# Optimization experiments

Measured on AMD Instinct MI355X. Metric: run time of the kernel, lower is better.

The kernel has to match this reference:

```python
import jax, jax.numpy as jnp
import numpy as np

H = 2048        # hidden_size
NH = 32         # num_attention_heads
HD = H // NH    # head_dim
I = 8192        # intermediate_size
L = 2           # num_hidden_layers
B, S = 1, 2048
EPS = 1e-5


def _layernorm(x, gamma):
    # keras LayerNormalization(center=False): mean-subtract, var-normalize, scale by gamma (no beta)
    mu = jnp.mean(x, axis=-1, keepdims=True)
    var = jnp.mean(jnp.square(x - mu), axis=-1, keepdims=True)
    return (x - mu) * jax.lax.rsqrt(var + EPS) * gamma


def _gelu_tanh(x):
    return 0.5 * x * (1.0 + jnp.tanh(0.7978845608028654 * x * (1.0 + 0.044715 * x * x)))


def setup_inputs() -> dict:
    key = jax.random.key(0)
    ks = jax.random.split(key, 12)
    sd = 0.02
    inputs_embeds = jax.random.normal(ks[0], (B, S, H), dtype=jnp.float32)
    attention_mask = jnp.tril(jnp.ones((S, S), dtype=bool))[None, None]  # causal [1,1,S,S]
    return {
        "inputs_embeds": inputs_embeds,
        "attention_mask": attention_mask,
        "Wq": jax.random.normal(ks[1], (L, H, H), jnp.float32) * sd,
        "Wk": jax.random.normal(ks[2], (L, H, H), jnp.float32) * sd,
        "Wv": jax.random.normal(ks[3], (L, H, H), jnp.float32) * sd,
        "Wo": jax.random.normal(ks[4], (L, H, H), jnp.float32) * sd,
        "bo": jnp.zeros((L, H), jnp.float32),
        "W1": jax.random.normal(ks[5], (L, H, I), jnp.float32) * sd,
        "W2": jax.random.normal(ks[6], (L, I, H), jnp.float32) * sd,
        "b2": jnp.zeros((L, H), jnp.float32),
        "g1": jnp.ones((L, H), jnp.float32),
        "g2": jnp.ones((L, H), jnp.float32),
        "gf": jnp.ones((H,), jnp.float32),
    }


def _forward(inputs_embeds, attention_mask, Wq, Wk, Wv, Wo, bo, W1, W2, b2, g1, g2, gf):
    x = inputs_embeds
    scale = 1.0 / jnp.sqrt(jnp.float32(HD))
    for l in range(L):
        # --- attention block ---
        h = _layernorm(x, g1[l])
        q = h @ Wq[l]
        k = h @ Wk[l]
        v = h @ Wv[l]
        # split heads: [B,S,H] -> [B,NH,S,HD]
        q = q.reshape(B, S, NH, HD).transpose(0, 2, 1, 3)
        k = k.reshape(B, S, NH, HD).transpose(0, 2, 1, 3)
        v = v.reshape(B, S, NH, HD).transpose(0, 2, 1, 3)
        scores = jnp.einsum("bhqd,bhkd->bhqk", q, k) * scale
        scores = jnp.where(attention_mask, scores, jnp.float32(-1e9))
        probs = jax.nn.softmax(scores, axis=-1)
        ctx = jnp.einsum("bhqk,bhkd->bhqd", probs, v)
        ctx = ctx.transpose(0, 2, 1, 3).reshape(B, S, H)
        x = x + (ctx @ Wo[l] + bo[l])
        # --- MLP block ---
        h = _layernorm(x, g2[l])
        h = _gelu_tanh(h @ W1[l]) @ W2[l] + b2[l]
        x = x + h
    return _layernorm(x, gf)


def reference(inputs_embeds, attention_mask, Wq, Wk, Wv, Wo, bo, W1, W2, b2, g1, g2, gf):
    return _forward(inputs_embeds, attention_mask, Wq, Wk, Wv, Wo, bo, W1, W2, b2, g1, g2, gf)
```

## Files before the change

### kernel.cpp

```cpp
#include <hip/hip_runtime.h>
#include <hip/hip_bf16.h>
#include <stdint.h>


#define H_   2048
#define NH_  32
#define HD_  64
#define I_   8192
#define L_   2
#define S_   2048
#define EPS_ 1e-5f

typedef _Float16 f16;
typedef __attribute__((ext_vector_type(8))) _Float16 f16x8;
typedef __attribute__((ext_vector_type(4))) float   f32x4;

#define BF16_PROBE 0x3F803F80u

static __device__ __forceinline__ float bf2f(unsigned short b) {
  return __uint_as_float(((unsigned int)b) << 16);
}

static __device__ __forceinline__ float gelu_f(float x) {
  float y = 0.7978845608028654f * x * (1.0f + 0.044715f * x * x);
  return x / (1.0f + __expf(-2.0f * y));
}

#define GLDS(gp, lp)                                                          \
  __builtin_amdgcn_global_load_lds(                                           \
      (const __attribute__((address_space(1))) unsigned int*)(gp),            \
      (__attribute__((address_space(3))) unsigned int*)(lp), 16, 0, 0)

__global__ __launch_bounds__(256) void embed2f_k(const void* __restrict__ e,
                                                 float* __restrict__ xf,
                                                 const unsigned int* __restrict__ probe) {
  bool isbf = (*probe == BF16_PROBE);
  int i = (blockIdx.x * 256 + threadIdx.x) * 4;
  float4 o;
  if (isbf) {
    uint2 d = *(const uint2*)((const unsigned short*)e + i);
    o.x = bf2f((unsigned short)(d.x & 0xffff));
    o.y = bf2f((unsigned short)(d.x >> 16));
    o.z = bf2f((unsigned short)(d.y & 0xffff));
    o.w = bf2f((unsigned short)(d.y >> 16));
  } else {
    o = *(const float4*)((const float*)e + i);
  }
  *(float4*)(xf + i) = o;
}

template <int OUT_FINAL>
__global__ __launch_bounds__(256) void ln_k(const float* __restrict__ x,
                                            const void* __restrict__ gammav,
                                            size_t geoff,
                                            void* __restrict__ outv,
                                            const unsigned int* __restrict__ probe) {
  bool isbf = (*probe == BF16_PROBE);
  int row = blockIdx.x, t = threadIdx.x;
  const float* xr = x + (size_t)row * H_;
  float4 a = ((const float4*)xr)[t];
  float4 b = ((const float4*)xr)[t + 256];
  float s  = a.x + a.y + a.z + a.w + b.x + b.y + b.z + b.w;
  float ss = a.x*a.x + a.y*a.y + a.z*a.z + a.w*a.w
           + b.x*b.x + b.y*b.y + b.z*b.z + b.w*b.w;
#pragma unroll
  for (int m = 32; m >= 1; m >>= 1) { s += __shfl_xor(s, m); ss += __shfl_xor(ss, m); }
  __shared__ float red[8];
  if ((t & 63) == 0) { red[t >> 6] = s; red[4 + (t >> 6)] = ss; }
  __syncthreads();
  s  = red[0] + red[1] + red[2] + red[3];
  ss = red[4] + red[5] + red[6] + red[7];
  float mu   = s * (1.0f / H_);
  float rstd = rsqrtf(ss * (1.0f / H_) - mu * mu + EPS_);
  float va[8] = {a.x, a.y, a.z, a.w, b.x, b.y, b.z, b.w};
#pragma unroll
  for (int hh = 0; hh < 2; ++hh) {
    int cbase = (hh == 0) ? t * 4 : (t + 256) * 4;
#pragma unroll
    for (int j = 0; j < 4; ++j) {
      int c = cbase + j;
      float g = isbf ? bf2f(((const unsigned short*)gammav)[geoff + c])
                     : ((const float*)gammav)[geoff + c];
      float o = (va[hh * 4 + j] - mu) * rstd * g;
      size_t idx = (size_t)row * H_ + c;
      if (OUT_FINAL) {
        if (isbf) ((__hip_bfloat16*)outv)[idx] = __float2bfloat16(o);
        else      ((float*)outv)[idx] = o;
      } else {
        ((f16*)outv)[idx] = (f16)o;
      }
    }
  }
}

__global__ __launch_bounds__(256) void transp_k(const void* __restrict__ in,
                                                size_t eoff,
                                                f16* __restrict__ out, int R, int C,
                                                const unsigned int* __restrict__ probe) {
  bool isbf = (*probe == BF16_PROBE);
  __shared__ __attribute__((aligned(16))) f16 tile[64][72];
  int t = threadIdx.x;
  int r0 = blockIdx.y * 64, c0 = blockIdx.x * 64;
#pragma unroll
  for (int it = 0; it < 2; ++it) {
    int idx = it * 256 + t;
    int r = idx >> 3, c8 = (idx & 7) * 8;
    size_t goff = eoff + (size_t)(r0 + r) * C + c0 + c8;
    if (isbf) {
      uint4 d = *(const uint4*)((const unsigned short*)in + goff);
      unsigned int dw[4] = {d.x, d.y, d.z, d.w};
#pragma unroll
      for (int p = 0; p < 4; ++p) {
        tile[r][c8 + 2 * p]     = (f16)bf2f((unsigned short)(dw[p] & 0xffff));
        tile[r][c8 + 2 * p + 1] = (f16)bf2f((unsigned short)(dw[p] >> 16));
      }
    } else {
      float4 fa = *(const float4*)((const float*)in + goff);
      float4 fb = *(const float4*)((const float*)in + goff + 4);
      tile[r][c8 + 0] = (f16)fa.x; tile[r][c8 + 1] = (f16)fa.y;
      tile[r][c8 + 2] = (f16)fa.z; tile[r][c8 + 3] = (f16)fa.w;
      tile[r][c8 + 4] = (f16)fb.x; tile[r][c8 + 5] = (f16)fb.y;
      tile[r][c8 + 6] = (f16)fb.z; tile[r][c8 + 7] = (f16)fb.w;
    }
  }
  __syncthreads();
#pragma unroll
  for (int it = 0; it < 2; ++it) {
    int idx = it * 256 + t;
    int rn = idx >> 3, k8 = (idx & 7) * 8;
    f16x8 o;
#pragma unroll
    for (int j = 0; j < 8; ++j) o[j] = tile[k8 + j][rn];
    *(f16x8*)(out + (size_t)(c0 + rn) * R + r0 + k8) = o;
  }
}


#define MIDBAR()                                                              \
  asm volatile("" ::: "memory");                                              \
  __builtin_amdgcn_s_barrier();                                               \
  asm volatile("s_waitcnt lgkmcnt(0)" ::: "memory");                          \
  __builtin_amdgcn_sched_barrier(0);                                          \
  __builtin_amdgcn_s_setprio(1)

#define ENDBAR()                                                              \
  asm volatile("" ::: "memory");                                              \
  __builtin_amdgcn_s_barrier();                                               \
  __builtin_amdgcn_sched_barrier(0)

#define LDA8(AF, BUF, MH)                                                     \
  _Pragma("unroll") for (int m2 = 0; m2 < 4; ++m2)                            \
  _Pragma("unroll") for (int kk = 0; kk < 2; ++kk)                            \
    AF[m2][kk] = *(const f16x8*)(lds + (BUF) * 32768 +                        \
        (wr * 128 + (MH) * 64 + m2 * 16 + col) * 64 +                         \
        ((((kk << 2) + quad) ^ xq) << 3));

#define LDB4(BF, BUF, NH)                                                     \
  _Pragma("unroll") for (int n2 = 0; n2 < 2; ++n2)                            \
  _Pragma("unroll") for (int kk = 0; kk < 2; ++kk)                            \
    BF[n2][kk] = *(const f16x8*)(lds + 16384 + (BUF) * 32768 +                \
        (wc * 64 + (NH) * 32 + n2 * 16 + col) * 64 +                         \
        ((((kk << 2) + quad) ^ xq) << 3));

#define QMM(AF, BF, MH, NH)                                                   \
  _Pragma("unroll") for (int m2 = 0; m2 < 4; ++m2)                            \
  _Pragma("unroll") for (int n2 = 0; n2 < 2; ++n2)                            \
  _Pragma("unroll") for (int kk = 0; kk < 2; ++kk)                            \
    acc[(MH) * 4 + m2][(NH) * 2 + n2] =                                       \
        __builtin_amdgcn_mfma_f32_16x16x32_f16(                               \
            AF[m2][kk], BF[n2][kk], acc[(MH) * 4 + m2][(NH) * 2 + n2], 0, 0, 0);

template <int MODE>
__global__ __launch_bounds__(512, 2) void gemm256_k(const f16* __restrict__ A,
                                                    const f16* __restrict__ Bt,
                                                    f16* __restrict__ Cf,
                                                    float* __restrict__ xres,
                                                    const void* __restrict__ biasv,
                                                    size_t beoff,
                                                    int N, int K,
                                                    const unsigned int* __restrict__ probe) {
  __shared__ __attribute__((aligned(16))) f16 lds[65536];
  const int t = threadIdx.x;
  const int lane = t & 63, wid = t >> 6;
  const int col = lane & 15, quad = lane >> 4;
  const int xq = lane & 7;
  const int wr = wid >> 2, wc = wid & 3;
  const int tm = blockIdx.x * 256, tn = blockIdx.y * 256;
  const int KSP = K / (int)gridDim.z;
  const int kb  = (int)blockIdx.z * KSP;
  const int NK  = KSP >> 6;

  f32x4 acc[8][4];
#pragma unroll
  for (int i = 0; i < 8; ++i)
#pragma unroll
    for (int j = 0; j < 4; ++j) acc[i][j] = (f32x4){0.f, 0.f, 0.f, 0.f};

  const int srow = t >> 3;
  const int gs   = (t & 7) ^ (srow & 7);
  const f16* gA = A  + (size_t)(tm + srow) * K + kb + gs * 8;
  const f16* gB = Bt + (size_t)(tn + srow) * K + kb + gs * 8;
  f16* lbase = lds + t * 8;

  auto STAGE = [&](int mat, int h, int u) {
    if (u >= NK) return;
    const f16* gp0 = (mat ? gB : gA) + (size_t)(h * 128) * K + u * 64;
    f16* lp = lbase + (u & 1) * 32768 + mat * 16384 + h * 8192;
    GLDS(gp0, lp);
    GLDS(gp0 + (size_t)64 * K, lp + 4096);
  };

  STAGE(1, 0, 0); STAGE(1, 1, 0); STAGE(0, 0, 0); STAGE(0, 1, 0);
  STAGE(1, 0, 1); STAGE(1, 1, 1);
  asm volatile("s_waitcnt vmcnt(4)" ::: "memory");
  __builtin_amdgcn_s_barrier();
  __builtin_amdgcn_sched_barrier(0);

  f16x8 afr[4][2], b0f[2][2], b1f[2][2];

  for (int u = 0; u < NK; ++u) {
    const int b = u & 1;
    LDA8(afr, b, 0);
    LDB4(b0f, b, 0);
    STAGE(0, 0, u + 1);
    MIDBAR();
    QMM(afr, b0f, 0, 0);
    __builtin_amdgcn_s_setprio(0);
    ENDBAR();
    LDB4(b1f, b, 1);
    STAGE(0, 1, u + 1);
    MIDBAR();
    QMM(afr, b1f, 0, 1);
    __builtin_amdgcn_s_setprio(0);
    ENDBAR();
    LDA8(afr, b, 1);
    STAGE(1, 0, u + 2);
    MIDBAR();
    QMM(afr, b1f, 1, 1);
    __builtin_amdgcn_s_setprio(0);
    ENDBAR();
    STAGE(1, 1, u + 2);
    MIDBAR();
    QMM(afr, b0f, 1, 0);
    __builtin_amdgcn_s_setprio(0);
    if (u + 2 < NK) { asm volatile("s_waitcnt vmcnt(4)" ::: "memory"); }
    else            { asm volatile("s_waitcnt vmcnt(0)" ::: "memory"); }
    ENDBAR();
  }

  bool isbf = false;
  if (MODE == 2) isbf = (*probe == BF16_PROBE);
  const bool addb = (MODE == 2) && (blockIdx.z == 0);
#pragma unroll
  for (int m = 0; m < 8; ++m) {
    int row = tm + wr * 128 + m * 16 + quad * 4;
#pragma unroll
    for (int n = 0; n < 4; ++n) {
      int cg = tn + wc * 64 + n * 16 + col;
#pragma unroll
      for (int r = 0; r < 4; ++r) {
        float v = acc[m][n][r];
        if (MODE == 1) v = gelu_f(v);
        size_t idx = (size_t)(row + r) * N + cg;
        if (MODE <= 1) {
          Cf[idx] = (f16)v;
        } else {
          if (addb) {
            v += isbf ? bf2f(((const unsigned short*)biasv)[beoff + cg])
                      : ((const float*)biasv)[beoff + cg];
          }
          atomicAdd(xres + idx, v);
        }
      }
    }
  }
}

__global__ __launch_bounds__(256) void attn_k(const f16* __restrict__ qkv,
                                              f16* __restrict__ ctx) {
  __shared__ __attribute__((aligned(16))) f16 Ks[64 * 72];
  __shared__ __attribute__((aligned(16))) f16 Vt[64 * 72];
  __shared__ __attribute__((aligned(16))) f16 Ps[4 * 16 * 72];
  const int RS = 3 * H_;
  int t = threadIdx.x, w = t >> 6, lane = t & 63;
  int col = lane & 15, quad = lane >> 4;
  int head = blockIdx.y;
  int qt = (gridDim.x - 1) - blockIdx.x;
  int q0 = qt * 64;

  int qrow = q0 + w * 16 + col;
  const f16* qp = qkv + (size_t)qrow * RS + head * HD_ + quad * 8;
  f16x8 qf0 = *(const f16x8*)qp;
  f16x8 qf1 = *(const f16x8*)(qp + 32);

  f32x4 O[4];
#pragma unroll
  for (int ht = 0; ht < 4; ++ht) O[ht] = (f32x4){0.f, 0.f, 0.f, 0.f};
  f32x4 mrow = (f32x4){-1e30f, -1e30f, -1e30f, -1e30f};
  f32x4 lrow = (f32x4){0.f, 0.f, 0.f, 0.f};
  f16* pw = Ps + w * 16 * 72;

  for (int c = 0; c <= qt; ++c) {
    int k0 = c * 64;
#pragma unroll
    for (int it = 0; it < 2; ++it) {
      int idx = it * 256 + t;
      int r = idx >> 3, c8 = (idx & 7) * 8;
      const f16* kp = qkv + (size_t)(k0 + r) * RS + H_ + head * HD_ + c8;
      *(f16x8*)(Ks + r * 72 + c8) = *(const f16x8*)kp;
      const f16* vp = qkv + (size_t)(k0 + r) * RS + 2 * H_ + head * HD_ + c8;
      f16x8 vv = *(const f16x8*)vp;
#pragma unroll
      for (int j = 0; j < 8; ++j) Vt[(c8 + j) * 72 + r] = vv[j];
    }
    __syncthreads();

    f32x4 s[4];
#pragma unroll
    for (int nt = 0; nt < 4; ++nt) {
      const f16* kb = Ks + (nt * 16 + col) * 72 + quad * 8;
      f16x8 b0 = *(const f16x8*)kb;
      f16x8 b1 = *(const f16x8*)(kb + 32);
      f32x4 z = (f32x4){0.f, 0.f, 0.f, 0.f};
      z = __builtin_amdgcn_mfma_f32_16x16x32_f16(qf0, b0, z, 0, 0, 0);
      z = __builtin_amdgcn_mfma_f32_16x16x32_f16(qf1, b1, z, 0, 0, 0);
      s[nt] = z;
    }
    int rq = q0 + w * 16 + quad * 4;
#pragma unroll
    for (int nt = 0; nt < 4; ++nt)
#pragma unroll
      for (int r = 0; r < 4; ++r) {
        float sv = s[nt][r] * 0.125f;
        if (k0 + nt * 16 + col > rq + r) sv = -1e30f;
        s[nt][r] = sv;
      }
    f32x4 mx;
#pragma unroll
    for (int r = 0; r < 4; ++r)
      mx[r] = fmaxf(fmaxf(s[0][r], s[1][r]), fmaxf(s[2][r], s[3][r]));
#pragma unroll
    for (int m = 1; m <= 8; m <<= 1)
#pragma unroll
      for (int r = 0; r < 4; ++r) mx[r] = fmaxf(mx[r], __shfl_xor(mx[r], m));
    f32x4 mnew, alpha, rs;
#pragma unroll
    for (int r = 0; r < 4; ++r) {
      mnew[r]  = fmaxf(mrow[r], mx[r]);
      alpha[r] = __expf(mrow[r] - mnew[r]);
      rs[r] = 0.f;
    }
#pragma unroll
    for (int nt = 0; nt < 4; ++nt)
#pragma unroll
      for (int r = 0; r < 4; ++r) {
        float p = __expf(s[nt][r] - mnew[r]);
        s[nt][r] = p;
        rs[r] += p;
      }
#pragma unroll
    for (int m = 1; m <= 8; m <<= 1)
#pragma unroll
      for (int r = 0; r < 4; ++r) rs[r] += __shfl_xor(rs[r], m);
#pragma unroll
    for (int r = 0; r < 4; ++r) {
      lrow[r] = lrow[r] * alpha[r] + rs[r];
      mrow[r] = mnew[r];
    }
#pragma unroll
    for (int ht = 0; ht < 4; ++ht)
#pragma unroll
      for (int r = 0; r < 4; ++r) O[ht][r] *= alpha[r];

#pragma unroll
    for (int nt = 0; nt < 4; ++nt)
#pragma unroll
      for (int r = 0; r < 4; ++r)
        pw[(quad * 4 + r) * 72 + nt * 16 + col] = (f16)s[nt][r];
    const f16* pr = pw + col * 72 + quad * 8;
    f16x8 p0 = *(const f16x8*)pr;
    f16x8 p1 = *(const f16x8*)(pr + 32);
#pragma unroll
    for (int ht = 0; ht < 4; ++ht) {
      const f16* vb = Vt + (ht * 16 + col) * 72 + quad * 8;
      f16x8 v0 = *(const f16x8*)vb;
      f16x8 v1 = *(const f16x8*)(vb + 32);
      O[ht] = __builtin_amdgcn_mfma_f32_16x16x32_f16(p0, v0, O[ht], 0, 0, 0);
      O[ht] = __builtin_amdgcn_mfma_f32_16x16x32_f16(p1, v1, O[ht], 0, 0, 0);
    }
    __syncthreads();
  }

#pragma unroll
  for (int ht = 0; ht < 4; ++ht)
#pragma unroll
    for (int r = 0; r < 4; ++r) {
      int row = q0 + w * 16 + quad * 4 + r;
      int cg = head * HD_ + ht * 16 + col;
      ctx[(size_t)row * H_ + cg] = (f16)(O[ht][r] / lrow[r]);
    }
}

extern "C" void kernel_launch(void* const* d_in, const int* in_sizes, int n_in,
                              void* d_out, int out_size, void* d_ws, size_t ws_size,
                              hipStream_t stream) {
  const void* embeds = d_in[0];
  const void* Wq = d_in[2];
  const void* Wk = d_in[3];
  const void* Wv = d_in[4];
  const void* Wo = d_in[5];
  const void* bo = d_in[6];
  const void* W1 = d_in[7];
  const void* W2 = d_in[8];
  const void* b2 = d_in[9];
  const void* g1 = d_in[10];
  const void* g2 = d_in[11];
  const void* gf = d_in[12];
  const unsigned int* probe = (const unsigned int*)g1;

  char* W = (char*)d_ws;
  float* xf  = (float*)(W);
  f16* hbuf  = (f16*)(W + (16ull << 20));
  f16* qkvb  = (f16*)(W + (24ull << 20));
  f16* ctxb  = (f16*)(W + (48ull << 20));
  f16* m1b   = (f16*)(W + (24ull << 20));
  f16* Wt    = (f16*)(W + (56ull << 20));
  (void)in_sizes; (void)n_in; (void)out_size; (void)ws_size;

  embed2f_k<<<S_ * H_ / 1024, 256, 0, stream>>>(embeds, xf, probe);

  for (int l = 0; l < L_; ++l) {
    size_t wo = (size_t)l * H_ * H_;
    ln_k<0><<<S_, 256, 0, stream>>>(xf, g1, (size_t)l * H_, hbuf, probe);
    transp_k<<<dim3(H_ / 64, H_ / 64), 256, 0, stream>>>(Wq, wo, Wt, H_, H_, probe);
    transp_k<<<dim3(H_ / 64, H_ / 64), 256, 0, stream>>>(Wk, wo, Wt + (size_t)H_ * H_, H_, H_, probe);
    transp_k<<<dim3(H_ / 64, H_ / 64), 256, 0, stream>>>(Wv, wo, Wt + 2ull * H_ * H_, H_, H_, probe);
    gemm256_k<0><<<dim3(S_ / 256, 3 * H_ / 256), 512, 0, stream>>>(hbuf, Wt, qkvb, nullptr, nullptr, 0, 3 * H_, H_, probe);
    attn_k<<<dim3(S_ / 64, NH_), 256, 0, stream>>>(qkvb, ctxb);
    transp_k<<<dim3(H_ / 64, H_ / 64), 256, 0, stream>>>(Wo, wo, Wt, H_, H_, probe);
    gemm256_k<2><<<dim3(S_ / 256, H_ / 256, 4), 512, 0, stream>>>(ctxb, Wt, nullptr, xf, bo, (size_t)l * H_, H_, H_, probe);
    ln_k<0><<<S_, 256, 0, stream>>>(xf, g2, (size_t)l * H_, hbuf, probe);
    transp_k<<<dim3(I_ / 64, H_ / 64), 256, 0, stream>>>(W1, (size_t)l * H_ * I_, Wt, H_, I_, probe);
    gemm256_k<1><<<dim3(S_ / 256, I_ / 256), 512, 0, stream>>>(hbuf, Wt, m1b, nullptr, nullptr, 0, I_, H_, probe);
    transp_k<<<dim3(H_ / 64, I_ / 64), 256, 0, stream>>>(W2, (size_t)l * I_ * H_, Wt, I_, H_, probe);
    gemm256_k<2><<<dim3(S_ / 256, H_ / 256, 4), 512, 0, stream>>>(m1b, Wt, nullptr, xf, b2, (size_t)l * H_, H_, I_, probe);
  }
  ln_k<1><<<S_, 256, 0, stream>>>(xf, gf, 0, d_out, probe);
}
```

Before: 1.522 ms.

## Double-buffer attention K/V tiles with 128-query blocks and stagger split-K GEMM tiles

```diff
diff --git a/kernel.cpp b/kernel.cpp
--- a/kernel.cpp
+++ b/kernel.cpp
@@ -185,7 +185,10 @@
   const int col = lane & 15, quad = lane >> 4;
   const int xq = lane & 7;
   const int wr = wid >> 2, wc = wid & 3;
-  const int tm = blockIdx.x * 256, tn = blockIdx.y * 256;
+  const int tm = blockIdx.x * 256;
+  int yy = (int)blockIdx.y + (int)blockIdx.z;
+  if (yy >= (int)gridDim.y) yy -= (int)gridDim.y;
+  const int tn = yy * 256;
   const int KSP = K / (int)gridDim.z;
   const int kb  = (int)blockIdx.z * KSP;
   const int NK  = KSP >> 6;
@@ -276,117 +279,133 @@
   }
 }
 
-__global__ __launch_bounds__(256) void attn_k(const f16* __restrict__ qkv,
+__global__ __launch_bounds__(512) void attn_k(const f16* __restrict__ qkv,
                                               f16* __restrict__ ctx) {
-  __shared__ __attribute__((aligned(16))) f16 Ks[64 * 72];
-  __shared__ __attribute__((aligned(16))) f16 Vt[64 * 72];
-  __shared__ __attribute__((aligned(16))) f16 Ps[4 * 16 * 72];
+  __shared__ __attribute__((aligned(16))) f16 Ks[2][64 * 64];
+  __shared__ __attribute__((aligned(16))) f16 Vt[2][64 * 72];
+  __shared__ __attribute__((aligned(16))) f16 Ps[8][16 * 72];
   const int RS = 3 * H_;
   int t = threadIdx.x, w = t >> 6, lane = t & 63;
   int col = lane & 15, quad = lane >> 4;
   int head = blockIdx.y;
-  int qt = (gridDim.x - 1) - blockIdx.x;
-  int q0 = qt * 64;
+  int qb = (gridDim.x - 1) - blockIdx.x;
+  int q0 = qb * 128;
+  const int NC = qb * 2 + 2;
 
   int qrow = q0 + w * 16 + col;
   const f16* qp = qkv + (size_t)qrow * RS + head * HD_ + quad * 8;
   f16x8 qf0 = *(const f16x8*)qp;
   f16x8 qf1 = *(const f16x8*)(qp + 32);
 
+  const int sr = t >> 3, sg = t & 7;
+  const f16* kgp = qkv + (size_t)sr * RS + H_ + head * HD_ + ((sg ^ (sr & 7)) * 8);
+  const f16* vgp = qkv + (size_t)sr * RS + 2 * H_ + head * HD_ + sg * 8;
+  f16* klp = &Ks[0][0] + t * 8;
+
   f32x4 O[4];
 #pragma unroll
   for (int ht = 0; ht < 4; ++ht) O[ht] = (f32x4){0.f, 0.f, 0.f, 0.f};
   f32x4 mrow = (f32x4){-1e30f, -1e30f, -1e30f, -1e30f};
   f32x4 lrow = (f32x4){0.f, 0.f, 0.f, 0.f};
-  f16* pw = Ps + w * 16 * 72;
-
-  for (int c = 0; c <= qt; ++c) {
-    int k0 = c * 64;
-#pragma unroll
-    for (int it = 0; it < 2; ++it) {
-      int idx = it * 256 + t;
-      int r = idx >> 3, c8 = (idx & 7) * 8;
-      const f16* kp = qkv + (size_t)(k0 + r) * RS + H_ + head * HD_ + c8;
-      *(f16x8*)(Ks + r * 72 + c8) = *(const f16x8*)kp;
-      const f16* vp = qkv + (size_t)(k0 + r) * RS + 2 * H_ + head * HD_ + c8;
-      f16x8 vv = *(const f16x8*)vp;
-#pragma unroll
-      for (int j = 0; j < 8; ++j) Vt[(c8 + j) * 72 + r] = vv[j];
-    }
-    __syncthreads();
-
-    f32x4 s[4];
-#pragma unroll
-    for (int nt = 0; nt < 4; ++nt) {
-      const f16* kb = Ks + (nt * 16 + col) * 72 + quad * 8;
-      f16x8 b0 = *(const f16x8*)kb;
-      f16x8 b1 = *(const f16x8*)(kb + 32);
-      f32x4 z = (f32x4){0.f, 0.f, 0.f, 0.f};
-      z = __builtin_amdgcn_mfma_f32_16x16x32_f16(qf0, b0, z, 0, 0, 0);
-      z = __builtin_amdgcn_mfma_f32_16x16x32_f16(qf1, b1, z, 0, 0, 0);
-      s[nt] = z;
-    }
-    int rq = q0 + w * 16 + quad * 4;
-#pragma unroll
-    for (int nt = 0; nt < 4; ++nt)
+  f16* pw = &Ps[w][0];
+
+  GLDS(kgp, klp);
+  f16x8 vv = *(const f16x8*)vgp;
+#pragma unroll
+  for (int j = 0; j < 8; ++j) Vt[0][(sg * 8 + j) * 72 + sr] = vv[j];
+  __syncthreads();
+
+  for (int c = 0; c < NC; ++c) {
+    const int b = c & 1;
+    if (c + 1 < NC) {
+      size_t roff = (size_t)(c + 1) * 64 * RS;
+      GLDS(kgp + roff, klp + (1 - b) * 64 * 64);
+      vv = *(const f16x8*)(vgp + roff);
+    }
+
+    const bool active = (c * 64 <= q0 + w * 16 + 15);
+    if (active) {
+      int k0 = c * 64;
+      f32x4 s[4];
+#pragma unroll
+      for (int nt = 0; nt < 4; ++nt) {
+        int key = nt * 16 + col;
+        const f16* kb0 = &Ks[b][key * 64 + ((quad ^ (key & 7)) * 8)];
+        const f16* kb1 = &Ks[b][key * 64 + (((quad + 4) ^ (key & 7)) * 8)];
+        f16x8 b0 = *(const f16x8*)kb0;
+        f16x8 b1 = *(const f16x8*)kb1;
+        f32x4 z = (f32x4){0.f, 0.f, 0.f, 0.f};
+        z = __builtin_amdgcn_mfma_f32_16x16x32_f16(qf0, b0, z, 0, 0, 0);
+        z = __builtin_amdgcn_mfma_f32_16x16x32_f16(qf1, b1, z, 0, 0, 0);
+        s[nt] = z;
+      }
+      int rq = q0 + w * 16 + quad * 4;
+#pragma unroll
+      for (int nt = 0; nt < 4; ++nt)
+#pragma unroll
+        for (int r = 0; r < 4; ++r) {
+          float sv = s[nt][r] * 0.125f;
+          if (k0 + nt * 16 + col > rq + r) sv = -1e30f;
+          s[nt][r] = sv;
+        }
+      f32x4 mx;
+#pragma unroll
+      for (int r = 0; r < 4; ++r)
+        mx[r] = fmaxf(fmaxf(s[0][r], s[1][r]), fmaxf(s[2][r], s[3][r]));
+#pragma unroll
+      for (int m = 1; m <= 8; m <<= 1)
+#pragma unroll
+        for (int r = 0; r < 4; ++r) mx[r] = fmaxf(mx[r], __shfl_xor(mx[r], m));
+      f32x4 mnew, alpha, rs;
 #pragma unroll
       for (int r = 0; r < 4; ++r) {
-        float sv = s[nt][r] * 0.125f;
-        if (k0 + nt * 16 + col > rq + r) sv = -1e30f;
-        s[nt][r] = sv;
-      }
-    f32x4 mx;
-#pragma unroll
-    for (int r = 0; r < 4; ++r)
-      mx[r] = fmaxf(fmaxf(s[0][r], s[1][r]), fmaxf(s[2][r], s[3][r]));
-#pragma unroll
-    for (int m = 1; m <= 8; m <<= 1)
-#pragma unroll
-      for (int r = 0; r < 4; ++r) mx[r] = fmaxf(mx[r], __shfl_xor(mx[r], m));
-    f32x4 mnew, alpha, rs;
-#pragma unroll
-    for (int r = 0; r < 4; ++r) {
-      mnew[r]  = fmaxf(mrow[r], mx[r]);
-      alpha[r] = __expf(mrow[r] - mnew[r]);
-      rs[r] = 0.f;
-    }
-#pragma unroll
-    for (int nt = 0; nt < 4; ++nt)
+        mnew[r]  = fmaxf(mrow[r], mx[r]);
+        alpha[r] = __expf(mrow[r] - mnew[r]);
+        rs[r] = 0.f;
+      }
+#pragma unroll
+      for (int nt = 0; nt < 4; ++nt)
+#pragma unroll
+        for (int r = 0; r < 4; ++r) {
+          float p = __expf(s[nt][r] - mnew[r]);
+          s[nt][r] = p;
+          rs[r] += p;
+        }
+#pragma unroll
+      for (int m = 1; m <= 8; m <<= 1)
+#pragma unroll
+        for (int r = 0; r < 4; ++r) rs[r] += __shfl_xor(rs[r], m);
 #pragma unroll
       for (int r = 0; r < 4; ++r) {
-        float p = __expf(s[nt][r] - mnew[r]);
-        s[nt][r] = p;
-        rs[r] += p;
-      }
-#pragma unroll
-    for (int m = 1; m <= 8; m <<= 1)
-#pragma unroll
-      for (int r = 0; r < 4; ++r) rs[r] += __shfl_xor(rs[r], m);
-#pragma unroll
-    for (int r = 0; r < 4; ++r) {
-      lrow[r] = lrow[r] * alpha[r] + rs[r];
-      mrow[r] = mnew[r];
-    }
-#pragma unroll
-    for (int ht = 0; ht < 4; ++ht)
-#pragma unroll
-      for (int r = 0; r < 4; ++r) O[ht][r] *= alpha[r];
-
-#pragma unroll
-    for (int nt = 0; nt < 4; ++nt)
-#pragma unroll
-      for (int r = 0; r < 4; ++r)
-        pw[(quad * 4 + r) * 72 + nt * 16 + col] = (f16)s[nt][r];
-    const f16* pr = pw + col * 72 + quad * 8;
-    f16x8 p0 = *(const f16x8*)pr;
-    f16x8 p1 = *(const f16x8*)(pr + 32);
-#pragma unroll
-    for (int ht = 0; ht < 4; ++ht) {
-      const f16* vb = Vt + (ht * 16 + col) * 72 + quad * 8;
-      f16x8 v0 = *(const f16x8*)vb;
-      f16x8 v1 = *(const f16x8*)(vb + 32);
-      O[ht] = __builtin_amdgcn_mfma_f32_16x16x32_f16(p0, v0, O[ht], 0, 0, 0);
-      O[ht] = __builtin_amdgcn_mfma_f32_16x16x32_f16(p1, v1, O[ht], 0, 0, 0);
+        lrow[r] = lrow[r] * alpha[r] + rs[r];
+        mrow[r] = mnew[r];
+      }
+#pragma unroll
+      for (int ht = 0; ht < 4; ++ht)
+#pragma unroll
+        for (int r = 0; r < 4; ++r) O[ht][r] *= alpha[r];
+
+#pragma unroll
+      for (int nt = 0; nt < 4; ++nt)
+#pragma unroll
+        for (int r = 0; r < 4; ++r)
+          pw[(quad * 4 + r) * 72 + nt * 16 + col] = (f16)s[nt][r];
+      const f16* pr = pw + col * 72 + quad * 8;
+      f16x8 p0 = *(const f16x8*)pr;
+      f16x8 p1 = *(const f16x8*)(pr + 32);
+#pragma unroll
+      for (int ht = 0; ht < 4; ++ht) {
+        const f16* vb = &Vt[b][(ht * 16 + col) * 72 + quad * 8];
+        f16x8 v0 = *(const f16x8*)vb;
+        f16x8 v1 = *(const f16x8*)(vb + 32);
+        O[ht] = __builtin_amdgcn_mfma_f32_16x16x32_f16(p0, v0, O[ht], 0, 0, 0);
+        O[ht] = __builtin_amdgcn_mfma_f32_16x16x32_f16(p1, v1, O[ht], 0, 0, 0);
+      }
+    }
+
+    if (c + 1 < NC) {
+#pragma unroll
+      for (int j = 0; j < 8; ++j) Vt[1 - b][(sg * 8 + j) * 72 + sr] = vv[j];
     }
     __syncthreads();
   }
@@ -436,7 +455,7 @@
     transp_k<<<dim3(H_ / 64, H_ / 64), 256, 0, stream>>>(Wk, wo, Wt + (size_t)H_ * H_, H_, H_, probe);
     transp_k<<<dim3(H_ / 64, H_ / 64), 256, 0, stream>>>(Wv, wo, Wt + 2ull * H_ * H_, H_, H_, probe);
     gemm256_k<0><<<dim3(S_ / 256, 3 * H_ / 256), 512, 0, stream>>>(hbuf, Wt, qkvb, nullptr, nullptr, 0, 3 * H_, H_, probe);
-    attn_k<<<dim3(S_ / 64, NH_), 256, 0, stream>>>(qkvb, ctxb);
+    attn_k<<<dim3(S_ / 128, NH_), 512, 0, stream>>>(qkvb, ctxb);
     transp_k<<<dim3(H_ / 64, H_ / 64), 256, 0, stream>>>(Wo, wo, Wt, H_, H_, probe);
     gemm256_k<2><<<dim3(S_ / 256, H_ / 256, 4), 512, 0, stream>>>(ctxb, Wt, nullptr, xf, bo, (size_t)l * H_, H_, H_, probe);
     ln_k<0><<<S_, 256, 0, stream>>>(xf, g2, (size_t)l * H_, hbuf, probe);
```

New measurement: 1.439 ms. -5.5%, faster.
